# Kernel optimization log

Measured on AMD Instinct MI355X. Metric: run time of the kernel, lower is better.

The kernel has to match this reference:

```python
import jax, jax.numpy as jnp
import numpy as np

B, S, D, L = 8, 512, 768, 200


def leaky(x, slope=0.2):
    return jnp.where(x >= 0, x, slope * x)


def l1_normalize(x, axis):
    # torch.nn.functional.normalize(p=1): x / max(sum|x|, 1e-12)
    return x / jnp.maximum(jnp.sum(jnp.abs(x), axis=axis, keepdims=True), 1e-12)


def setup_inputs() -> dict:
    key = jax.random.key(0)
    ks = jax.random.split(key, 16)
    s = 1.0 / np.sqrt(D)
    return {
        "doc_embedding": jax.random.normal(ks[0], (B, S, D), jnp.float32),
        "labels": jax.random.uniform(ks[1], (B, L), jnp.float32),
        "label_embed": jax.random.normal(ks[2], (L, D), jnp.float32),
        "label_adj": jax.random.uniform(ks[3], (L, L), jnp.float32),
        "w_gcn3": jax.random.uniform(ks[4], (D, D), jnp.float32, -s, s),
        "w_gcn5": jax.random.uniform(ks[5], (D, D), jnp.float32, -s, s),
        "w_ll1": jax.random.normal(ks[6], (D, D), jnp.float32) * s,
        "b_ll1": jax.random.normal(ks[7], (D,), jnp.float32) * s,
        "w_ll2": jax.random.normal(ks[8], (D, D), jnp.float32) * s,
        "b_ll2": jax.random.normal(ks[9], (D,), jnp.float32) * s,
        "w_lin": jax.random.normal(ks[10], (2 * D, D), jnp.float32) * (1.0 / np.sqrt(2 * D)),
        "b_lin": jax.random.normal(ks[11], (D,), jnp.float32) * s,
        "conv_w": jax.random.normal(ks[12], (L, 1, 9, 9), jnp.float32) * (1.0 / 9.0),
        "conv_b": jax.random.normal(ks[13], (L,), jnp.float32) * 0.01,
        "w_lin1": jax.random.normal(ks[14], (D, L), jnp.float32) * s,
        "b_lin1": jax.random.normal(ks[15], (L,), jnp.float32) * s,
    }


def reference(doc_embedding, labels, label_embed, label_adj, w_gcn3, w_gcn5,
              w_ll1, b_ll1, w_ll2, b_ll2, w_lin, b_lin, conv_w, conv_b,
              w_lin1, b_lin1):
    b = doc_embedding.shape[0]
    # stacked (replicated) label embeddings: [B, L, D]
    le = jnp.broadcast_to(label_embed, (b,) + label_embed.shape)

    # GCN3: adj @ (x @ W), leaky relu 0.2
    le = leaky(jnp.einsum('lm,bmd->bld', label_adj, le @ w_gcn3))

    # learned adjacency A = sigmoid(lin1(le) @ lin2(le)^T)   [B, L, L]
    q = le @ w_ll1 + b_ll1
    k = le @ w_ll2 + b_ll2
    A = jax.nn.sigmoid(jnp.einsum('bld,bmd->blm', q, k))

    # normalize_adj: D^{-1/2} with detached row sum; out = (A D)^T D
    row_sum = jax.lax.stop_gradient(jnp.sum(A, axis=1))  # [B, L]
    d_inv_sqrt = jnp.where(row_sum > 0, row_sum ** -0.5, 0.0)
    AD = A * d_inv_sqrt[:, None, :]                 # A @ diag(d)
    A_norm = jnp.swapaxes(AD, 1, 2) * d_inv_sqrt[:, None, :]

    # GCN5 with learned adj
    d_le = leaky(jnp.einsum('blm,bmd->bld', A_norm, le @ w_gcn5))

    le_cat = jnp.concatenate([le, d_le], axis=-1)   # [B, L, 2D]
    le_out = le_cat @ w_lin + b_lin                 # [B, L, D]

    le_out = l1_normalize(le_out, axis=-2)
    doc = l1_normalize(doc_embedding, axis=-2)

    # word-label attention map [B, S, L]
    wla = jnp.einsum('bsd,bld->bsl', doc, le_out)

    # conv2d 1 -> L channels, 9x9, pad 4 over [B, 1, S, L]
    att = jax.lax.conv_general_dilated(
        wla[:, None, :, :], conv_w, window_strides=(1, 1),
        padding=((4, 4), (4, 4)),
        dimension_numbers=('NCHW', 'OIHW', 'NCHW'))
    att = att + conv_b[None, :, None, None]         # [B, L, S, L]

    att = jnp.max(att, axis=1)                      # [B, S, L]
    att = jnp.max(att, axis=-1, keepdims=True)      # [B, S, 1]
    gate = jnp.tanh(att)

    h_enc = jnp.sum(gate * doc, axis=1)             # [B, D]
    label_output = jax.nn.sigmoid(h_enc @ w_lin1 + b_lin1)

    eps = 1e-7
    p = jnp.clip(label_output, eps, 1.0 - eps)
    loss = -jnp.mean(labels * jnp.log(p) + (1.0 - labels) * jnp.log(1.0 - p))
    return label_output, loss
```

## Files before the change

kernel.cpp:

```cpp
#include <hip/hip_runtime.h>
#include <hip/hip_bf16.h>
#include <math.h>

#define BB 8
#define SS 512
#define DD 768
#define LL 200

typedef __attribute__((ext_vector_type(8))) short bf16x8;
typedef __attribute__((ext_vector_type(4))) float f32x4;

__device__ inline short f2bf(float f) {
    unsigned u = __builtin_bit_cast(unsigned, f);
    unsigned r = (u + 0x7FFFu + ((u >> 16) & 1u)) >> 16;
    return (short)r;
}
__device__ inline float bf2f(short s) {
    unsigned u = ((unsigned)(unsigned short)s) << 16;
    return __builtin_bit_cast(float, u);
}

#define LDP3 264
#define BK3  256
#define MGLDS (2 * 64 * LDP3 * 2)

template<int EPI, bool TB>
__global__ __launch_bounds__(256, 1) void mgemm_k(
    const short* __restrict__ A, int lda,
    const void* __restrict__ Bv, int ldb,
    const float* __restrict__ bias,
    const void* __restrict__ Bv2, const float* __restrict__ bias2, int nsplit,
    const void* __restrict__ Bv3, const float* __restrict__ bias3, int nsplit2,
    float* __restrict__ Cf, int ldc,
    short* __restrict__ Cb, int ldcb,
    short* __restrict__ Ct, int ldct, int nsplitT,
    int M, int N, int K)
{
    extern __shared__ short dsm[];
    short* As = dsm;
    short* Bs = dsm + 64 * LDP3;
    const int tid = threadIdx.x;
    const int bm = blockIdx.y * 64;
    const int bn = blockIdx.x * 64;
    int bnb = bn;
    if (!TB) {
        if (bn >= nsplit2)      { Bv = Bv3; bias = bias3; bnb = bn - nsplit2; }
        else if (bn >= nsplit)  { Bv = Bv2; bias = bias2; bnb = bn - nsplit; }
    }
    const int w = tid >> 6, lane = tid & 63, g = lane >> 4, ln = lane & 15;
    const int Kp = (K + BK3 - 1) & ~(BK3 - 1);
    const int nt = Kp >> 8;

    const int ar = tid >> 2, ac = tid & 3;
    const int bn_ = tid & 63, bko = (tid >> 6) * 64;

    f32x4 acc[4];
    #pragma unroll
    for (int i = 0; i < 4; ++i) acc[i] = (f32x4){0.f, 0.f, 0.f, 0.f};

    bf16x8 aR[8], bT[8];
    #pragma unroll
    for (int j = 0; j < 8; ++j) { aR[j] = (bf16x8){0,0,0,0,0,0,0,0}; bT[j] = (bf16x8){0,0,0,0,0,0,0,0}; }
    float bF[64];
    #pragma unroll
    for (int j = 0; j < 64; ++j) bF[j] = 0.f;

    const int gmS = bm + ar;
    const bool aOk = (gmS < M);

    auto fetchA = [&](int k0) {
        if (aOk) {
            const short* p = A + (size_t)gmS * lda + k0 + ac * 64;
            #pragma unroll
            for (int j = 0; j < 8; ++j) aR[j] = *(const bf16x8*)(p + j * 8);
        }
    };
    auto fetchB = [&](int k0) {
        if (TB) {
            const short* Bt = (const short*)Bv;
            int gn = bn + ar;
            if (gn < N) {
                const short* p = Bt + (size_t)gn * ldb + k0 + ac * 64;
                #pragma unroll
                for (int j = 0; j < 8; ++j) bT[j] = *(const bf16x8*)(p + j * 8);
            }
        } else {
            const float* Bp = (const float*)Bv + (size_t)(bnb + bn_);
            #pragma unroll
            for (int j = 0; j < 64; ++j) {
                int gk = k0 + bko + j;
                bF[j] = (gk < K) ? Bp[(size_t)gk * ldb] : 0.f;
            }
        }
    };

    fetchA(0);
    fetchB(0);

    for (int t = 0; t < nt; ++t) {
        {
            short* pa = As + ar * LDP3 + ac * 64;
            #pragma unroll
            for (int j = 0; j < 8; ++j) *(bf16x8*)(pa + j * 8) = aR[j];
        }
        if (TB) {
            short* pb = Bs + ar * LDP3 + ac * 64;
            #pragma unroll
            for (int j = 0; j < 8; ++j) *(bf16x8*)(pb + j * 8) = bT[j];
        } else {
            short* pb = Bs + bn_ * LDP3 + bko;
            #pragma unroll
            for (int q = 0; q < 8; ++q) {
                bf16x8 v;
                #pragma unroll
                for (int e = 0; e < 8; ++e) v[e] = f2bf(bF[q * 8 + e]);
                *(bf16x8*)(pb + q * 8) = v;
            }
        }
        __syncthreads();

        if (t + 1 < nt) {
            int k0 = (t + 1) << 8;
            fetchA(k0);
            fetchB(k0);
        }

        #pragma unroll
        for (int ks = 0; ks < 8; ++ks) {
            bf16x8 a = *(const bf16x8*)(As + (w * 16 + ln) * LDP3 + ks * 32 + g * 8);
            #pragma unroll
            for (int nb = 0; nb < 4; ++nb) {
                bf16x8 b = *(const bf16x8*)(Bs + (nb * 16 + ln) * LDP3 + ks * 32 + g * 8);
                acc[nb] = __builtin_amdgcn_mfma_f32_16x16x32_bf16(a, b, acc[nb], 0, 0, 0);
            }
        }
        __syncthreads();
    }

    #pragma unroll
    for (int nb = 0; nb < 4; ++nb) {
        int gn = bn + nb * 16 + ln;
        float bv = (bias && gn < N) ? bias[bnb + nb * 16 + ln] : 0.f;
        #pragma unroll
        for (int r = 0; r < 4; ++r) {
            int gm = bm + w * 16 + g * 4 + r;
            if (gm < M && gn < N) {
                float v = acc[nb][r] + bv;
                if (EPI == 1) v = (v >= 0.f) ? v : 0.2f * v;
                else if (EPI == 2) v = 1.f / (1.f + expf(-v));
                if (Cf) Cf[(size_t)gm * ldc + gn] = v;
                if (Cb) Cb[(size_t)gm * ldcb + gn] = f2bf(v);
                if (Ct && gn >= nsplitT)
                    Ct[(size_t)(gn - nsplitT) * ldct + gm] = f2bf(v);
            }
        }
    }
}

#define WP 168
#define TP 24
#define WTR 217
#define WROWS 208
#define APAD 256
#define BIGN (1 << 30)

__global__ void prep_k(const float* __restrict__ cw, const float* __restrict__ cb,
                       const float* __restrict__ adj,
                       short* __restrict__ wkg, short* __restrict__ adj_bf)
{
    int idx = blockIdx.x * blockDim.x + threadIdx.x;
    if (idx < WROWS * WP) {
        int o = idx / WP, kk = idx % WP;
        int kj = kk >> 4, ki = kk & 15;
        float v = 0.f;
        if (o < LL && kj < 9) {
            if (ki < 9) v = cw[o * 81 + ki * 9 + kj];
            else if (ki == 9 && kj == 0) v = cb[o];
        }
        wkg[idx] = f2bf(v);
        return;
    }
    idx -= WROWS * WP;
    if (idx < LL * APAD) {
        int r = idx / APAD, c = idx % APAD;
        adj_bf[idx] = f2bf(c < LL ? adj[r * LL + c] : 0.f);
    }
}

__global__ void ca_k(const float* __restrict__ A, short* __restrict__ An)
{
    int i = blockIdx.x;
    int j = threadIdx.x;
    float si = 0.f, sj = 0.f;
    for (int l = 0; l < LL; ++l) {
        si += A[l * LL + i];
        if (j < LL) sj += A[l * LL + j];
    }
    float di = (si > 0.f) ? (1.f / sqrtf(si)) : 0.f;
    float dj = (sj > 0.f) ? (1.f / sqrtf(sj)) : 0.f;
    float v = (j < LL) ? A[j * LL + i] * di * dj : 0.f;
    An[i * APAD + j] = f2bf(v);
}

__global__ void l1n_k(const float* __restrict__ X, short* __restrict__ Xb)
{
    int c = threadIdx.x >> 5, r = threadIdx.x & 31;
    int col = blockIdx.x * 8 + c;
    float s = 0.f;
    for (int l = r; l < LL; l += 32) s += fabsf(X[l * DD + col]);
    #pragma unroll
    for (int off = 16; off > 0; off >>= 1) s += __shfl_xor(s, off, 64);
    float inv = 1.f / fmaxf(s, 1e-12f);
    for (int l = r; l < LL; l += 32)
        Xb[l * DD + col] = f2bf(X[l * DD + col] * inv);
}

__global__ void docsumA_k(const float* __restrict__ doc, float* __restrict__ dpart)
{
    int dc = blockIdx.x, sc = blockIdx.y, b = blockIdx.z;
    int dx = threadIdx.x & 63, sy = threadIdx.x >> 6;
    int d = dc * 64 + dx;
    const float* pp = doc + ((size_t)b * SS + sc * 64) * DD + d;
    float s = 0.f;
    for (int t = sy; t < 64; t += 4) s += fabsf(pp[(size_t)t * DD]);
    __shared__ float red[4][64];
    red[sy][dx] = s;
    __syncthreads();
    if (sy == 0)
        dpart[((size_t)b * 8 + sc) * DD + d] = red[0][dx] + red[1][dx] + red[2][dx] + red[3][dx];
}

__global__ void docbfB_k(const float* __restrict__ doc, const float* __restrict__ dpart,
                         short* __restrict__ docb)
{
    int gid = blockIdx.x * blockDim.x + threadIdx.x;
    if (gid >= BB * SS * DD / 4) return;
    size_t base = (size_t)gid * 4;
    int d = (int)(base % DD);
    int b = (int)(base / ((size_t)SS * DD));
    float4 v = *(const float4*)(doc + base);
    float4 dn = {0.f, 0.f, 0.f, 0.f};
    #pragma unroll
    for (int sc = 0; sc < 8; ++sc) {
        float4 t = *(const float4*)(dpart + ((size_t)b * 8 + sc) * DD + d);
        dn.x += t.x; dn.y += t.y; dn.z += t.z; dn.w += t.w;
    }
    dn.x = fmaxf(dn.x, 1e-12f); dn.y = fmaxf(dn.y, 1e-12f);
    dn.z = fmaxf(dn.z, 1e-12f); dn.w = fmaxf(dn.w, 1e-12f);
    short4 o;
    o.x = f2bf(v.x / dn.x);
    o.y = f2bf(v.y / dn.y);
    o.z = f2bf(v.z / dn.z);
    o.w = f2bf(v.w / dn.w);
    *(short4*)(docb + base) = o;
}

template<int NS>
__device__ __forceinline__ void conv_body2(const short* __restrict__ Wlh,
                                           const short* __restrict__ WT,
                                           int lrow0, int soffG,
                                           int ln, int g, float& lm)
{
    bf16x8 Af[NS][5];
    #pragma unroll
    for (int s = 0; s < NS; ++s)
        #pragma unroll
        for (int j = 0; j < 5; ++j)
            Af[s][j] = *(const bf16x8*)(Wlh + (lrow0 + s * 16 + ln) * WP + j * 32 + g * 8);

    #pragma unroll 1
    for (int nt = 0; nt < 13; ++nt) {
        bf16x8 Bf[5];
        #pragma unroll
        for (int j = 0; j < 5; ++j)
            Bf[j] = *(const bf16x8*)(WT + (nt * 16 + ln + 2 * j + (g >> 1)) * TP + (g & 1) * 8);

        f32x4 acc[NS];
        #pragma unroll
        for (int s = 0; s < NS; ++s) acc[s] = (f32x4){0.f, 0.f, 0.f, 0.f};

        #pragma unroll
        for (int j = 0; j < 5; ++j)
            #pragma unroll
            for (int s = 0; s < NS; ++s)
                acc[s] = __builtin_amdgcn_mfma_f32_16x16x32_bf16(Af[s][j], Bf[j], acc[s], 0, 0, 0);

        bool colOK = (nt < 12) | (ln < 8);
        #pragma unroll
        for (int s = 0; s < NS; ++s) {
            float t = fmaxf(fmaxf(acc[s][0], acc[s][1]), fmaxf(acc[s][2], acc[s][3]));
            bool ok = colOK & ((soffG + s < 12) | (g < 2));
            lm = ok ? fmaxf(lm, t) : lm;
        }
    }
}

__global__ __launch_bounds__(512, 2) void conv_max_k(
    const float* __restrict__ wla,
    const short* __restrict__ wkg,
    float* __restrict__ ghalf)
{
    extern __shared__ short smem[];
    short* Wlh  = smem;
    short* winT = Wlh + 112 * WP;
    __shared__ float wredf[8];

    const int blk = blockIdx.x;
    const int h = blk & 1;
    const int sg = (blk >> 1) & 127;
    const int b = blk >> 8;
    const int s0 = sg << 2;
    const int tid = threadIdx.x;

    {
        const int4* src = (const int4*)wkg;
        int4* dst = (int4*)Wlh;
        const int row0 = h * 112;
        for (int i = tid; i < 112 * 21; i += 512) {
            int r = i / 21, c = i % 21;
            int gr = row0 + r;
            int4 v = {0, 0, 0, 0};
            if (gr < WROWS) v = src[gr * 21 + c];
            dst[i] = v;
        }
    }
    for (int idx = tid; idx < 4 * WTR; idx += 512) {
        int p = idx / WTR, r = idx % WTR;
        int col = r - 4;
        short vals[16];
        #pragma unroll
        for (int i = 0; i < 9; ++i) {
            int srow = s0 + p - 4 + i;
            float v = 0.f;
            if (srow >= 0 && srow < SS && col >= 0 && col < LL)
                v = wla[((size_t)b * SS + srow) * LL + col];
            vals[i] = f2bf(v);
        }
        vals[9] = (short)0x3F80;
        #pragma unroll
        for (int i = 10; i < 16; ++i) vals[i] = 0;
        short* dstp = winT + (p * WTR + r) * TP;
        *(bf16x8*)dstp = *(const bf16x8*)vals;
        *(bf16x8*)(dstp + 8) = *(const bf16x8*)(vals + 8);
    }
    __syncthreads();

    const int w = tid >> 6;
    const int p = w >> 1;
    const int q = w & 1;
    const int lane = tid & 63;
    const int g = lane >> 4;
    const int ln = lane & 15;
    const short* WT = winT + p * WTR * TP;

    float lm = -INFINITY;
    if (h == 0) {
        if (q == 0) conv_body2<4>(Wlh, WT, 0,  0,  ln, g, lm);
        else        conv_body2<3>(Wlh, WT, 64, 4,  ln, g, lm);
    } else {
        if (q == 0) conv_body2<3>(Wlh, WT, 0,  7,  ln, g, lm);
        else        conv_body2<3>(Wlh, WT, 48, 10, ln, g, lm);
    }

    #pragma unroll
    for (int off = 32; off > 0; off >>= 1)
        lm = fmaxf(lm, __shfl_xor(lm, off, 64));
    if (lane == 0) wredf[w] = lm;
    __syncthreads();
    if (tid < 4)
        ghalf[(size_t)h * (BB * SS) + ((size_t)b << 9) + s0 + tid] =
            fmaxf(wredf[2 * tid], wredf[2 * tid + 1]);
}

__global__ void henc_part_k(const short* __restrict__ doc_nb, const float* __restrict__ ghalf,
                            float* __restrict__ hpart)
{
    int dc = blockIdx.x, sc = blockIdx.y, b = blockIdx.z;
    int dx = threadIdx.x & 63, sy = threadIdx.x >> 6;
    int d = dc * 64 + dx;
    __shared__ float gsh[64];
    __shared__ float red[4][64];
    if (threadIdx.x < 64) {
        int srow = sc * 64 + threadIdx.x;
        size_t bs = (size_t)b * SS + srow;
        gsh[threadIdx.x] = tanhf(fmaxf(ghalf[bs], ghalf[(size_t)BB * SS + bs]));
    }
    __syncthreads();
    float s = 0.f;
    for (int t = sy; t < 64; t += 4) {
        int srow = sc * 64 + t;
        s = fmaf(bf2f(doc_nb[((size_t)b * SS + srow) * DD + d]), gsh[t], s);
    }
    red[sy][dx] = s;
    __syncthreads();
    if (sy == 0)
        hpart[((size_t)b * 8 + sc) * DD + d] = red[0][dx] + red[1][dx] + red[2][dx] + red[3][dx];
}

__global__ void final2_k(const float* __restrict__ hpart,
                         const float* __restrict__ W, const float* __restrict__ bias,
                         float* __restrict__ out)
{
    int b = blockIdx.x, tid = threadIdx.x;
    __shared__ float hb[DD];
    for (int idx = tid; idx < DD; idx += 256) {
        float s = 0.f;
        #pragma unroll
        for (int sc = 0; sc < 8; ++sc) s += hpart[((size_t)b * 8 + sc) * DD + idx];
        hb[idx] = s;
    }
    __syncthreads();
    int l = tid;
    if (l < LL) {
        float acc = bias[l];
        for (int d = 0; d < DD; ++d) acc = fmaf(hb[d], W[d * LL + l], acc);
        out[b * LL + l] = 1.f / (1.f + expf(-acc));
    }
}

__global__ void loss_k(const float* __restrict__ out, const float* __restrict__ labels,
                       float* __restrict__ loss_out)
{
    float s = 0.f;
    for (int i = threadIdx.x; i < BB * LL; i += 256) {
        float p = out[i];
        p = fminf(fmaxf(p, 1e-7f), 1.f - 1e-7f);
        float y = labels[i];
        s += y * logf(p) + (1.f - y) * logf(1.f - p);
    }
    #pragma unroll
    for (int off = 32; off > 0; off >>= 1) s += __shfl_down(s, off, 64);
    __shared__ float ws[4];
    if ((threadIdx.x & 63) == 0) ws[threadIdx.x >> 6] = s;
    __syncthreads();
    if (threadIdx.x == 0)
        loss_out[0] = -(ws[0] + ws[1] + ws[2] + ws[3]) / (float)(BB * LL);
}

static void mgemm(hipStream_t st, int epi, bool tb,
                  const short* A, int lda, const void* B, int ldb,
                  const float* bias,
                  const void* B2, const float* bias2, int nsplit,
                  const void* B3, const float* bias3, int nsplit2,
                  float* Cf, int ldc, short* Cb, int ldcb,
                  short* Ct, int ldct, int nsplitT,
                  int M, int N, int K)
{
    dim3 g((N + 63) / 64, (M + 63) / 64);
    #define LAUNCH(E, T) do { \
        (void)hipFuncSetAttribute((const void*)mgemm_k<E, T>, \
                                  hipFuncAttributeMaxDynamicSharedMemorySize, MGLDS); \
        mgemm_k<E, T><<<g, 256, MGLDS, st>>>(A, lda, B, ldb, bias, B2, bias2, nsplit, \
                                             B3, bias3, nsplit2, Cf, ldc, Cb, ldcb, \
                                             Ct, ldct, nsplitT, M, N, K); \
    } while (0)
    if (!tb) {
        if (epi == 0)      LAUNCH(0, false);
        else if (epi == 1) LAUNCH(1, false);
        else               LAUNCH(2, false);
    } else {
        if (epi == 0)      LAUNCH(0, true);
        else if (epi == 1) LAUNCH(1, true);
        else               LAUNCH(2, true);
    }
    #undef LAUNCH
}

extern "C" void kernel_launch(void* const* d_in, const int* in_sizes, int n_in,
                              void* d_out, int out_size, void* d_ws, size_t ws_size,
                              hipStream_t stream)
{
    const float* doc_emb   = (const float*)d_in[0];
    const float* labels    = (const float*)d_in[1];
    const float* label_emb = (const float*)d_in[2];
    const float* label_adj = (const float*)d_in[3];
    const float* w_gcn3    = (const float*)d_in[4];
    const float* w_gcn5    = (const float*)d_in[5];
    const float* w_ll1     = (const float*)d_in[6];
    const float* b_ll1     = (const float*)d_in[7];
    const float* w_ll2     = (const float*)d_in[8];
    const float* b_ll2     = (const float*)d_in[9];
    const float* w_lin     = (const float*)d_in[10];
    const float* b_lin     = (const float*)d_in[11];
    const float* conv_w    = (const float*)d_in[12];
    const float* conv_b    = (const float*)d_in[13];
    const float* w_lin1    = (const float*)d_in[14];
    const float* b_lin1    = (const float*)d_in[15];

    float* out = (float*)d_out;

    char* p = (char*)d_ws;
    auto alloc = [&](size_t bytes) { void* r = p; p += (bytes + 15) & ~(size_t)15; return r; };
    short* wkg       = (short*)alloc(WROWS * WP * 2);
    short* adj_bf    = (short*)alloc(200 * APAD * 2);
    short* E2_bf     = (short*)alloc(200 * 768 * 2);
    short* le_cat_bf = (short*)alloc(200 * 1536 * 2);
    short* qkh_bf    = (short*)alloc(200 * 2304 * 2);
    short* Ht        = (short*)alloc(768 * 256 * 2);
    float* Amat      = (float*)alloc(200 * 200 * 4);
    short* Anorm_bf  = (short*)alloc(200 * APAD * 2);
    float* le_out_f  = (float*)alloc(200 * 768 * 4);
    short* le_out_bf = (short*)alloc(200 * 768 * 2);
    float* dpart     = (float*)alloc(BB * 8 * DD * 4);
    short* doc_nb    = (short*)alloc((size_t)BB * SS * DD * 2);
    float* wla       = (float*)alloc((size_t)BB * SS * LL * 4);
    float* ghalf     = (float*)alloc(2 * BB * SS * 4);
    float* hpart     = (float*)alloc(BB * 8 * DD * 4);

    docsumA_k<<<dim3(12, 8, 8), 256, 0, stream>>>(doc_emb, dpart);
    docbfB_k<<<(BB * SS * DD / 4 + 255) / 256, 256, 0, stream>>>(doc_emb, dpart, doc_nb);
    prep_k<<<(WROWS * WP + LL * APAD + 255) / 256, 256, 0, stream>>>(
        conv_w, conv_b, label_adj, wkg, adj_bf);
    mgemm(stream, 0, false, adj_bf, APAD, label_emb, DD, nullptr,
          nullptr, nullptr, BIGN, nullptr, nullptr, BIGN,
          nullptr, 0, E2_bf, DD, nullptr, 0, BIGN, LL, DD, LL);
    mgemm(stream, 1, false, E2_bf, DD, w_gcn3, DD, nullptr,
          nullptr, nullptr, BIGN, nullptr, nullptr, BIGN,
          nullptr, 0, le_cat_bf, 1536, nullptr, 0, BIGN, LL, DD, DD);
    mgemm(stream, 0, false, le_cat_bf, 1536, w_ll1, DD, b_ll1,
          w_ll2, b_ll2, DD, w_gcn5, nullptr, 2 * DD,
          nullptr, 0, qkh_bf, 2304, Ht, 256, 2 * DD, LL, 3 * DD, DD);
    mgemm(stream, 2, true, qkh_bf, 2304, qkh_bf + DD, 2304, nullptr,
          nullptr, nullptr, BIGN, nullptr, nullptr, BIGN,
          Amat, LL, nullptr, 0, nullptr, 0, BIGN, LL, LL, DD);
    ca_k<<<LL, 256, 0, stream>>>(Amat, Anorm_bf);
    mgemm(stream, 1, true, Anorm_bf, APAD, Ht, 256, nullptr,
          nullptr, nullptr, BIGN, nullptr, nullptr, BIGN,
          nullptr, 0, le_cat_bf + DD, 1536, nullptr, 0, BIGN, LL, DD, LL);
    mgemm(stream, 0, false, le_cat_bf, 1536, w_lin, DD, b_lin,
          nullptr, nullptr, BIGN, nullptr, nullptr, BIGN,
          le_out_f, DD, nullptr, 0, nullptr, 0, BIGN, LL, DD, 2 * DD);
    l1n_k<<<96, 256, 0, stream>>>(le_out_f, le_out_bf);
    mgemm(stream, 0, true, doc_nb, DD, le_out_bf, DD, nullptr,
          nullptr, nullptr, BIGN, nullptr, nullptr, BIGN,
          wla, LL, nullptr, 0, nullptr, 0, BIGN, BB * SS, LL, DD);
    (void)hipFuncSetAttribute((const void*)conv_max_k,
                              hipFuncAttributeMaxDynamicSharedMemorySize, 79296);
    conv_max_k<<<2048, 512, 79296, stream>>>(wla, wkg, ghalf);
    henc_part_k<<<dim3(12, 8, 8), 256, 0, stream>>>(doc_nb, ghalf, hpart);
    final2_k<<<BB, 256, 0, stream>>>(hpart, w_lin1, b_lin1, out);
    loss_k<<<1, 256, 0, stream>>>(out, labels, out + BB * LL);
}
```

Measured before the change: 270.8 us.

## Fuse prep kernels, store attention map as bf16, merge loss into final kernel

Merges the doc column-sum kernel with the conv-weight/adjacency prep kernel into one launch, and folds the loss computation into the final sigmoid kernel using an atomic add after a memset. The word-label attention map is now written as bf16 by the GEMM, halving its size, and the conv kernel stages a 12-row window in shared memory before transposing it, instead of doing nine strided global reads per element. Together these remove launches and memory traffic. The costs are an extra memset, an atomic accumulation of the loss, and an extra shared-memory pass and sync in the conv kernel.

```diff
diff --git a/kernel.cpp b/kernel.cpp
--- a/kernel.cpp
+++ b/kernel.cpp
@@ -164,11 +164,27 @@
 #define APAD 256
 #define BIGN (1 << 30)
 
-__global__ void prep_k(const float* __restrict__ cw, const float* __restrict__ cb,
-                       const float* __restrict__ adj,
-                       short* __restrict__ wkg, short* __restrict__ adj_bf)
-{
-    int idx = blockIdx.x * blockDim.x + threadIdx.x;
+__global__ void prepdoc_k(const float* __restrict__ doc, float* __restrict__ dpart,
+                          const float* __restrict__ cw, const float* __restrict__ cb,
+                          const float* __restrict__ adj,
+                          short* __restrict__ wkg, short* __restrict__ adj_bf)
+{
+    if (blockIdx.x < 768) {
+        int u = blockIdx.x;
+        int dc = u % 12, sc = (u / 12) % 8, b = u / 96;
+        int dx = threadIdx.x & 63, sy = threadIdx.x >> 6;
+        int d = dc * 64 + dx;
+        const float* pp = doc + ((size_t)b * SS + sc * 64) * DD + d;
+        float s = 0.f;
+        for (int t = sy; t < 64; t += 4) s += fabsf(pp[(size_t)t * DD]);
+        __shared__ float red[4][64];
+        red[sy][dx] = s;
+        __syncthreads();
+        if (sy == 0)
+            dpart[((size_t)b * 8 + sc) * DD + d] = red[0][dx] + red[1][dx] + red[2][dx] + red[3][dx];
+        return;
+    }
+    int idx = (blockIdx.x - 768) * 256 + threadIdx.x;
     if (idx < WROWS * WP) {
         int o = idx / WP, kk = idx % WP;
         int kj = kk >> 4, ki = kk & 15;
@@ -185,49 +201,6 @@
         int r = idx / APAD, c = idx % APAD;
         adj_bf[idx] = f2bf(c < LL ? adj[r * LL + c] : 0.f);
     }
-}
-
-__global__ void ca_k(const float* __restrict__ A, short* __restrict__ An)
-{
-    int i = blockIdx.x;
-    int j = threadIdx.x;
-    float si = 0.f, sj = 0.f;
-    for (int l = 0; l < LL; ++l) {
-        si += A[l * LL + i];
-        if (j < LL) sj += A[l * LL + j];
-    }
-    float di = (si > 0.f) ? (1.f / sqrtf(si)) : 0.f;
-    float dj = (sj > 0.f) ? (1.f / sqrtf(sj)) : 0.f;
-    float v = (j < LL) ? A[j * LL + i] * di * dj : 0.f;
-    An[i * APAD + j] = f2bf(v);
-}
-
-__global__ void l1n_k(const float* __restrict__ X, short* __restrict__ Xb)
-{
-    int c = threadIdx.x >> 5, r = threadIdx.x & 31;
-    int col = blockIdx.x * 8 + c;
-    float s = 0.f;
-    for (int l = r; l < LL; l += 32) s += fabsf(X[l * DD + col]);
-    #pragma unroll
-    for (int off = 16; off > 0; off >>= 1) s += __shfl_xor(s, off, 64);
-    float inv = 1.f / fmaxf(s, 1e-12f);
-    for (int l = r; l < LL; l += 32)
-        Xb[l * DD + col] = f2bf(X[l * DD + col] * inv);
-}
-
-__global__ void docsumA_k(const float* __restrict__ doc, float* __restrict__ dpart)
-{
-    int dc = blockIdx.x, sc = blockIdx.y, b = blockIdx.z;
-    int dx = threadIdx.x & 63, sy = threadIdx.x >> 6;
-    int d = dc * 64 + dx;
-    const float* pp = doc + ((size_t)b * SS + sc * 64) * DD + d;
-    float s = 0.f;
-    for (int t = sy; t < 64; t += 4) s += fabsf(pp[(size_t)t * DD]);
-    __shared__ float red[4][64];
-    red[sy][dx] = s;
-    __syncthreads();
-    if (sy == 0)
-        dpart[((size_t)b * 8 + sc) * DD + d] = red[0][dx] + red[1][dx] + red[2][dx] + red[3][dx];
 }
 
 __global__ void docbfB_k(const float* __restrict__ doc, const float* __restrict__ dpart,
@@ -255,6 +228,34 @@
     *(short4*)(docb + base) = o;
 }
 
+__global__ void ca_k(const float* __restrict__ A, short* __restrict__ An)
+{
+    int i = blockIdx.x;
+    int j = threadIdx.x;
+    float si = 0.f, sj = 0.f;
+    for (int l = 0; l < LL; ++l) {
+        si += A[l * LL + i];
+        if (j < LL) sj += A[l * LL + j];
+    }
+    float di = (si > 0.f) ? (1.f / sqrtf(si)) : 0.f;
+    float dj = (sj > 0.f) ? (1.f / sqrtf(sj)) : 0.f;
+    float v = (j < LL) ? A[j * LL + i] * di * dj : 0.f;
+    An[i * APAD + j] = f2bf(v);
+}
+
+__global__ void l1n_k(const float* __restrict__ X, short* __restrict__ Xb)
+{
+    int c = threadIdx.x >> 5, r = threadIdx.x & 31;
+    int col = blockIdx.x * 8 + c;
+    float s = 0.f;
+    for (int l = r; l < LL; l += 32) s += fabsf(X[l * DD + col]);
+    #pragma unroll
+    for (int off = 16; off > 0; off >>= 1) s += __shfl_xor(s, off, 64);
+    float inv = 1.f / fmaxf(s, 1e-12f);
+    for (int l = r; l < LL; l += 32)
+        Xb[l * DD + col] = f2bf(X[l * DD + col] * inv);
+}
+
 template<int NS>
 __device__ __forceinline__ void conv_body2(const short* __restrict__ Wlh,
                                            const short* __restrict__ WT,
@@ -296,13 +297,14 @@
 }
 
 __global__ __launch_bounds__(512, 2) void conv_max_k(
-    const float* __restrict__ wla,
+    const short* __restrict__ wlab,
     const short* __restrict__ wkg,
     float* __restrict__ ghalf)
 {
     extern __shared__ short smem[];
     short* Wlh  = smem;
     short* winT = Wlh + 112 * WP;
+    short* wbf  = Wlh;
     __shared__ float wredf[8];
 
     const int blk = blockIdx.x;
@@ -312,6 +314,28 @@
     const int s0 = sg << 2;
     const int tid = threadIdx.x;
 
+    for (int idx = tid; idx < 12 * 216; idx += 512) {
+        int r = idx / 216, c = idx % 216;
+        int sr = s0 - 4 + r, col = c - 4;
+        short v = 0;
+        if (sr >= 0 && sr < SS && col >= 0 && col < LL)
+            v = wlab[((size_t)b * SS + sr) * LL + col];
+        wbf[idx] = v;
+    }
+    __syncthreads();
+    for (int idx = tid; idx < 4 * WTR; idx += 512) {
+        int p = idx / WTR, r = idx % WTR;
+        short vals[16];
+        #pragma unroll
+        for (int i = 0; i < 9; ++i) vals[i] = (r < 216) ? wbf[(p + i) * 216 + r] : (short)0;
+        vals[9] = (short)0x3F80;
+        #pragma unroll
+        for (int i = 10; i < 16; ++i) vals[i] = 0;
+        short* dstp = winT + (p * WTR + r) * TP;
+        *(bf16x8*)dstp = *(const bf16x8*)vals;
+        *(bf16x8*)(dstp + 8) = *(const bf16x8*)(vals + 8);
+    }
+    __syncthreads();
     {
         const int4* src = (const int4*)wkg;
         int4* dst = (int4*)Wlh;
@@ -324,25 +348,6 @@
             dst[i] = v;
         }
     }
-    for (int idx = tid; idx < 4 * WTR; idx += 512) {
-        int p = idx / WTR, r = idx % WTR;
-        int col = r - 4;
-        short vals[16];
-        #pragma unroll
-        for (int i = 0; i < 9; ++i) {
-            int srow = s0 + p - 4 + i;
-            float v = 0.f;
-            if (srow >= 0 && srow < SS && col >= 0 && col < LL)
-                v = wla[((size_t)b * SS + srow) * LL + col];
-            vals[i] = f2bf(v);
-        }
-        vals[9] = (short)0x3F80;
-        #pragma unroll
-        for (int i = 10; i < 16; ++i) vals[i] = 0;
-        short* dstp = winT + (p * WTR + r) * TP;
-        *(bf16x8*)dstp = *(const bf16x8*)vals;
-        *(bf16x8*)(dstp + 8) = *(const bf16x8*)(vals + 8);
-    }
     __syncthreads();
 
     const int w = tid >> 6;
@@ -397,12 +402,13 @@
         hpart[((size_t)b * 8 + sc) * DD + d] = red[0][dx] + red[1][dx] + red[2][dx] + red[3][dx];
 }
 
-__global__ void final2_k(const float* __restrict__ hpart,
+__global__ void final3_k(const float* __restrict__ hpart,
                          const float* __restrict__ W, const float* __restrict__ bias,
-                         float* __restrict__ out)
+                         const float* __restrict__ labels, float* __restrict__ out)
 {
     int b = blockIdx.x, tid = threadIdx.x;
     __shared__ float hb[DD];
+    __shared__ float ws4[4];
     for (int idx = tid; idx < DD; idx += 256) {
         float s = 0.f;
         #pragma unroll
@@ -411,30 +417,22 @@
     }
     __syncthreads();
     int l = tid;
+    float term = 0.f;
     if (l < LL) {
         float acc = bias[l];
         for (int d = 0; d < DD; ++d) acc = fmaf(hb[d], W[d * LL + l], acc);
-        out[b * LL + l] = 1.f / (1.f + expf(-acc));
-    }
-}
-
-__global__ void loss_k(const float* __restrict__ out, const float* __restrict__ labels,
-                       float* __restrict__ loss_out)
-{
-    float s = 0.f;
-    for (int i = threadIdx.x; i < BB * LL; i += 256) {
-        float p = out[i];
-        p = fminf(fmaxf(p, 1e-7f), 1.f - 1e-7f);
-        float y = labels[i];
-        s += y * logf(p) + (1.f - y) * logf(1.f - p);
-    }
-    #pragma unroll
-    for (int off = 32; off > 0; off >>= 1) s += __shfl_down(s, off, 64);
-    __shared__ float ws[4];
-    if ((threadIdx.x & 63) == 0) ws[threadIdx.x >> 6] = s;
-    __syncthreads();
-    if (threadIdx.x == 0)
-        loss_out[0] = -(ws[0] + ws[1] + ws[2] + ws[3]) / (float)(BB * LL);
+        float sig = 1.f / (1.f + expf(-acc));
+        out[b * LL + l] = sig;
+        float pp = fminf(fmaxf(sig, 1e-7f), 1.f - 1e-7f);
+        float y = labels[b * LL + l];
+        term = y * logf(pp) + (1.f - y) * logf(1.f - pp);
+    }
+    #pragma unroll
+    for (int off = 32; off > 0; off >>= 1) term += __shfl_down(term, off, 64);
+    if ((tid & 63) == 0) ws4[tid >> 6] = term;
+    __syncthreads();
+    if (tid == 0)
+        atomicAdd(out + BB * LL, -(ws4[0] + ws4[1] + ws4[2] + ws4[3]) / (float)(BB * LL));
 }
 
 static void mgemm(hipStream_t st, int epi, bool tb,
@@ -503,14 +501,15 @@
     short* le_out_bf = (short*)alloc(200 * 768 * 2);
     float* dpart     = (float*)alloc(BB * 8 * DD * 4);
     short* doc_nb    = (short*)alloc((size_t)BB * SS * DD * 2);
-    float* wla       = (float*)alloc((size_t)BB * SS * LL * 4);
+    short* wlab      = (short*)alloc((size_t)BB * SS * LL * 2);
     float* ghalf     = (float*)alloc(2 * BB * SS * 4);
     float* hpart     = (float*)alloc(BB * 8 * DD * 4);
 
-    docsumA_k<<<dim3(12, 8, 8), 256, 0, stream>>>(doc_emb, dpart);
+    hipMemsetAsync(out + BB * LL, 0, 4, stream);
+
+    prepdoc_k<<<768 + (WROWS * WP + LL * APAD + 255) / 256, 256, 0, stream>>>(
+        doc_emb, dpart, conv_w, conv_b, label_adj, wkg, adj_bf);
     docbfB_k<<<(BB * SS * DD / 4 + 255) / 256, 256, 0, stream>>>(doc_emb, dpart, doc_nb);
-    prep_k<<<(WROWS * WP + LL * APAD + 255) / 256, 256, 0, stream>>>(
-        conv_w, conv_b, label_adj, wkg, adj_bf);
     mgemm(stream, 0, false, adj_bf, APAD, label_emb, DD, nullptr,
           nullptr, nullptr, BIGN, nullptr, nullptr, BIGN,
           nullptr, 0, E2_bf, DD, nullptr, 0, BIGN, LL, DD, LL);
@@ -533,11 +532,10 @@
     l1n_k<<<96, 256, 0, stream>>>(le_out_f, le_out_bf);
     mgemm(stream, 0, true, doc_nb, DD, le_out_bf, DD, nullptr,
           nullptr, nullptr, BIGN, nullptr, nullptr, BIGN,
-          wla, LL, nullptr, 0, nullptr, 0, BIGN, BB * SS, LL, DD);
+          nullptr, 0, wlab, LL, nullptr, 0, BIGN, BB * SS, LL, DD);
     (void)hipFuncSetAttribute((const void*)conv_max_k,
                               hipFuncAttributeMaxDynamicSharedMemorySize, 79296);
-    conv_max_k<<<2048, 512, 79296, stream>>>(wla, wkg, ghalf);
+    conv_max_k<<<2048, 512, 79296, stream>>>(wlab, wkg, ghalf);
     henc_part_k<<<dim3(12, 8, 8), 256, 0, stream>>>(doc_nb, ghalf, hpart);
-    final2_k<<<BB, 256, 0, stream>>>(hpart, w_lin1, b_lin1, out);
-    loss_k<<<1, 256, 0, stream>>>(out, labels, out + BB * LL);
-}
+    final3_k<<<BB, 256, 0, stream>>>(hpart, w_lin1, b_lin1, labels, out);
+}
```

Result: no change. 273.0 us (+0.8%).
